# Performance work log

Measured on AMD Instinct MI355X. Metric: run time of the kernel, lower is better.

Reference implementation:

```python
import jax, jax.numpy as jnp
import numpy as np

B, N, D = 4, 8192, 128
H = 4 * D  # exp_factor * features
EPS = 1e-5


def layer_norm(x):
    # fresh nn.LayerNorm each call -> weight=1, bias=0 (no learned affine)
    mu = jnp.mean(x, axis=-1, keepdims=True)
    var = jnp.var(x, axis=-1, keepdims=True)
    return (x - mu) * jax.lax.rsqrt(var + EPS)


def setup_inputs() -> dict:
    key = jax.random.key(0)
    ks = jax.random.split(key, 8)
    x = jax.random.normal(ks[0], (B, N, D), dtype=jnp.float32)
    adj = jax.random.uniform(ks[1], (N, N), dtype=jnp.float32)
    attn_mask = jnp.ones((1,), dtype=jnp.int32)  # unused (torch masked_fill result discarded)
    pad_mask = jnp.ones((1,), dtype=jnp.int32)   # unused
    # FFN params (torch Linear default init scale ~ 1/sqrt(fan_in))
    w1 = jax.random.normal(ks[2], (D, H), dtype=jnp.float32) / np.sqrt(D)
    b1 = jnp.zeros((H,), dtype=jnp.float32)
    w2 = jax.random.normal(ks[3], (H, D), dtype=jnp.float32) / np.sqrt(H)
    b2 = jnp.zeros((D,), dtype=jnp.float32)
    return {"x": x, "adj": adj, "attn_mask": attn_mask, "pad_mask": pad_mask,
            "w1": w1, "b1": b1, "w2": w2, "b2": b2, "dim": 128}


def reference(x, adj, attn_mask, pad_mask, w1, b1, w2, b2, dim):
    # Sublayer 0: x + InrAwaSA(LN(x))
    h = layer_norm(x)                               # [B,N,D]
    # adj is provided -> scores = dense adj, shared across batch.
    # NOTE: masks are no-ops in the source (masked_fill not in-place).
    prob = jax.nn.softmax(adj, axis=-1)             # [N,N]
    attn_out = jnp.einsum('nm,bmd->bnd', prob, h)   # [B,N,D]
    x1 = x + attn_out
    # Sublayer 1: x1 + FFN(LN(x1))
    h1 = layer_norm(x1)
    ffn = jnp.maximum(h1 @ w1 + b1, 0.0) @ w2 + b2
    return x1 + ffn
```

## Files before the change

kernel.cpp:

```cpp
#include <hip/hip_runtime.h>
#include <hip/hip_bf16.h>

typedef __attribute__((ext_vector_type(8))) short bh8;
typedef __attribute__((ext_vector_type(4))) float fx4;
typedef __attribute__((ext_vector_type(8))) int i32x8;
typedef __attribute__((ext_vector_type(4))) int i32x4;

typedef const __attribute__((address_space(1))) unsigned int* gas_p;
typedef __attribute__((address_space(3))) unsigned int* las_p;

#define MFMA(a, b, c) __builtin_amdgcn_mfma_f32_16x16x32_bf16((a), (b), (c), 0, 0, 0)
#define MFMAS(a, b, c) __builtin_amdgcn_mfma_scale_f32_16x16x128_f8f6f4( \
    (a), (b), (c), 0, 0, 0, 0x7f7f7f7f, 0, 0x7f7f7f7f)

__device__ __forceinline__ unsigned short f2bf(float f) {
  unsigned u = __builtin_bit_cast(unsigned, f);
  u += 0x7fff + ((u >> 16) & 1);
  return (unsigned short)(u >> 16);
}

__device__ __forceinline__ float bflo2f(unsigned u) { return __builtin_bit_cast(float, u << 16); }

__device__ __forceinline__ void gld16(const void* g, void* l) {
  __builtin_amdgcn_global_load_lds((gas_p)g, (las_p)l, 16, 0, 0);
}

__global__ __launch_bounds__(256) void transpose_weights(const float* __restrict__ w1,
                                                         const float* __restrict__ w2,
                                                         unsigned short* __restrict__ w1t,
                                                         unsigned short* __restrict__ w2t) {
  const int tgl = blockIdx.x * 256 + threadIdx.x;
  { const int h = tgl >> 7, d = tgl & 127; w1t[tgl] = f2bf(w1[d * 512 + h]); }
  { const int d = tgl >> 9, h = tgl & 511; w2t[tgl] = f2bf(w2[h * 128 + d]); }
}

__global__ __launch_bounds__(256) void ln1_transpose(const float* __restrict__ x,
                                                     unsigned char* __restrict__ ht) {
  const int t = threadIdx.x, lane = t & 63, w = t >> 6;
  const int mt = blockIdx.x, b = blockIdx.y;
  __shared__ unsigned short tile[128 * 64];
  const float* xb = x + ((size_t)b * 8192 + (size_t)mt * 64) * 128;
  for (int it = 0; it < 16; ++it) {
    const int r = w * 16 + it;
    const float2 v = *(const float2*)(xb + r * 128 + lane * 2);
    float s = v.x + v.y, s2 = v.x * v.x + v.y * v.y;
    #pragma unroll
    for (int o = 1; o < 64; o <<= 1) { s += __shfl_xor(s, o); s2 += __shfl_xor(s2, o); }
    const float mean = s * 0.0078125f;
    const float var = s2 * 0.0078125f - mean * mean;
    const float rstd = rsqrtf(var + 1e-5f);
    const int mc = r >> 3, ml = r & 7;
    const int d0 = lane * 2, d1 = d0 + 1;
    tile[d0 * 64 + ((mc ^ (d0 & 7)) << 3) + ml] = f2bf((v.x - mean) * rstd);
    tile[d1 * 64 + ((mc ^ (d1 & 7)) << 3) + ml] = f2bf((v.y - mean) * rstd);
  }
  __syncthreads();
  unsigned char* hb = ht + (size_t)b * 128 * 8192 + (size_t)mt * 64;
  #pragma unroll
  for (int i = 0; i < 4; ++i) {
    const int idx = i * 256 + t;
    const int d = idx >> 3, mc = idx & 7;
    const bh8 vv = *(const bh8*)(tile + d * 64 + ((mc ^ (d & 7)) << 3));
    int lo = 0, hi = 0;
    lo = __builtin_amdgcn_cvt_pk_fp8_f32(bflo2f((unsigned short)vv[0]),
                                         bflo2f((unsigned short)vv[1]), lo, false);
    lo = __builtin_amdgcn_cvt_pk_fp8_f32(bflo2f((unsigned short)vv[2]),
                                         bflo2f((unsigned short)vv[3]), lo, true);
    hi = __builtin_amdgcn_cvt_pk_fp8_f32(bflo2f((unsigned short)vv[4]),
                                         bflo2f((unsigned short)vv[5]), hi, false);
    hi = __builtin_amdgcn_cvt_pk_fp8_f32(bflo2f((unsigned short)vv[6]),
                                         bflo2f((unsigned short)vv[7]), hi, true);
    *(uint2*)(hb + (size_t)d * 8192 + mc * 8) = (uint2){(unsigned)lo, (unsigned)hi};
  }
}

__global__ __launch_bounds__(256, 2) void fused_attn(const float* __restrict__ adj,
                                                     const unsigned char* __restrict__ ht,
                                                     unsigned short* __restrict__ pbuf,
                                                     float* __restrict__ sden) {
  const int tid = threadIdx.x, lane = tid & 63, wn = tid >> 6;
  const int mt = blockIdx.x, z = blockIdx.y;
  const int kbase = z * 2048;

  __shared__ unsigned char Al[64 * 128];

  fx4 acc[4][8];
  #pragma unroll
  for (int i = 0; i < 4; ++i)
    #pragma unroll
    for (int j = 0; j < 8; ++j) acc[i][j] = (fx4){0.f, 0.f, 0.f, 0.f};

  i32x8 afr[4];

  const int ar = tid >> 2, aq = tid & 3;
  const float* aroot = adj + (size_t)(mt * 64 + ar) * 8192 + kbase;
  float sacc = 0.f;
  float4 a4[8];
  unsigned pk[8];

  auto issueAdj = [&](int tau) {
    #pragma unroll
    for (int j = 0; j < 8; ++j)
      a4[j] = *(const float4*)(aroot + tau * 128 + j * 16 + aq * 4);
  };
  auto expCvt = [&]() {
    #pragma unroll
    for (int j = 0; j < 8; ++j) {
      const float e0 = __expf(a4[j].x), e1 = __expf(a4[j].y);
      const float e2 = __expf(a4[j].z), e3 = __expf(a4[j].w);
      sacc += (e0 + e1) + (e2 + e3);
      int d = 0;
      d = __builtin_amdgcn_cvt_pk_fp8_f32(e0, e1, d, false);
      d = __builtin_amdgcn_cvt_pk_fp8_f32(e2, e3, d, true);
      pk[j] = (unsigned)d;
    }
  };
  auto writeA = [&]() {
    #pragma unroll
    for (int j = 0; j < 8; ++j)
      *(unsigned*)&Al[ar * 128 + ((j ^ (ar & 7)) << 4) + aq * 4] = pk[j];
  };
  auto ldAall = [&]() {
    #pragma unroll
    for (int mf = 0; mf < 4; ++mf) {
      const int rr = mf * 16 + (lane & 15);
      const int gb = (lane >> 4) * 2;
      const unsigned char* base = &Al[rr * 128];
      const i32x4 lo = *(const i32x4*)(base + ((gb ^ (rr & 7)) << 4));
      const i32x4 hi = *(const i32x4*)(base + (((gb + 1) ^ (rr & 7)) << 4));
      afr[mf] = (i32x8){lo.x, lo.y, lo.z, lo.w, hi.x, hi.y, hi.z, hi.w};
    }
  };

  issueAdj(0);
  expCvt();
  writeA();
  asm volatile("s_waitcnt lgkmcnt(0)" ::: "memory");
  __builtin_amdgcn_sched_barrier(0);
  __builtin_amdgcn_s_barrier();
  __builtin_amdgcn_sched_barrier(0);

  for (int tt = 0; tt < 16; ++tt) {
    ldAall();
    if (tt < 15) issueAdj(tt + 1);
    asm volatile("s_waitcnt lgkmcnt(0)" ::: "memory");
    __builtin_amdgcn_sched_barrier(0);
    __builtin_amdgcn_s_barrier();
    __builtin_amdgcn_sched_barrier(0);

    const unsigned char* bb = ht + kbase + tt * 128 + (size_t)(lane >> 4) * 32;
    #pragma unroll
    for (int p = 0; p < 8; ++p) {
      const int c = wn * 128 + p * 16 + (lane & 15);
      const unsigned char* cb = bb + (size_t)c * 8192;
      const i32x4 blo = *(const i32x4*)(cb);
      const i32x4 bhi = *(const i32x4*)(cb + 16);
      const i32x8 bfr = (i32x8){blo.x, blo.y, blo.z, blo.w, bhi.x, bhi.y, bhi.z, bhi.w};
      #pragma unroll
      for (int mf = 0; mf < 4; ++mf)
        acc[mf][p] = MFMAS(afr[mf], bfr, acc[mf][p]);
    }

    if (tt < 15) {
      expCvt();
      writeA();
      asm volatile("s_waitcnt lgkmcnt(0)" ::: "memory");
      __builtin_amdgcn_sched_barrier(0);
    }
    __builtin_amdgcn_s_barrier();
    __builtin_amdgcn_sched_barrier(0);
  }

  sacc += __shfl_xor(sacc, 1);
  sacc += __shfl_xor(sacc, 2);
  if (aq == 0) sden[(size_t)z * 8192 + mt * 64 + ar] = sacc;

  unsigned short* po = pbuf + (size_t)z * 8192 * 512;
  #pragma unroll
  for (int mf = 0; mf < 4; ++mf)
    #pragma unroll
    for (int nf = 0; nf < 8; ++nf) {
      const int col = wn * 128 + nf * 16 + (lane & 15);
      #pragma unroll
      for (int q = 0; q < 4; ++q) {
        const int row = mt * 64 + mf * 16 + (lane >> 4) * 4 + q;
        po[(size_t)row * 512 + col] = f2bf(acc[mf][nf][q]);
      }
    }
}

#define SWZ16(ks, r) (((((ks) & 7) ^ ((r) & 7)) | ((ks) & 8)))
__global__ __launch_bounds__(512) void ln_ffn_kernel(const float* __restrict__ x,
                                                     const unsigned short* __restrict__ pbuf,
                                                     const float* __restrict__ sden,
                                                     const unsigned short* __restrict__ w1t,
                                                     const unsigned short* __restrict__ w2t,
                                                     const float* __restrict__ b1,
                                                     const float* __restrict__ b2,
                                                     float* __restrict__ out) {
  const int t = threadIdx.x, lane = t & 63, w = t >> 6;
  const int wr = w >> 1, wc = w & 1;
  const int row0 = blockIdx.x * 128;
  __shared__ unsigned short As[128 * 128];
  __shared__ unsigned short W1c[128 * 128];
  __shared__ unsigned short W2c[128 * 128];
  __shared__ unsigned short Ts[128 * 128];

  auto stageW1 = [&](int hc) {
    #pragma unroll
    for (int i = 0; i < 4; ++i) {
      const int idx = i * 512 + t;
      const int row = idx >> 4, kc = idx & 15;
      const int kcs = (kc & 8) | ((kc & 7) ^ (row & 7));
      gld16(w1t + (size_t)(hc * 128 + row) * 128 + kcs * 8, W1c + (idx & ~63) * 8);
    }
  };
  auto stageW2 = [&](int hc) {
    #pragma unroll
    for (int i = 0; i < 4; ++i) {
      const int idx = i * 512 + t;
      const int row = idx >> 4, kc = idx & 15;
      const int kcs = (kc & 8) | ((kc & 7) ^ (row & 7));
      gld16(w2t + (size_t)row * 512 + hc * 128 + kcs * 8, W2c + (idx & ~63) * 8);
    }
  };

  stageW1(0); stageW2(0);

  const int r = t >> 2, q = t & 3, c0 = q * 32;
  const int rowg = row0 + r;
  const int bb = rowg >> 13, nn = rowg & 8191;
  float xv[32];
  {
    const float den = sden[nn] + sden[8192 + nn] + sden[16384 + nn] + sden[24576 + nn];
    const float rinv = 1.f / den;
    const float* xp = x + (size_t)rowg * 128 + c0;
    #pragma unroll
    for (int j = 0; j < 8; ++j) {
      const float4 v4 = *(const float4*)(xp + 4 * j);
      xv[4 * j] = v4.x; xv[4 * j + 1] = v4.y; xv[4 * j + 2] = v4.z; xv[4 * j + 3] = v4.w;
    }
    #pragma unroll
    for (int z = 0; z < 4; ++z) {
      const unsigned short* pp = pbuf + ((size_t)z * 8192 + nn) * 512 + bb * 128 + c0;
      #pragma unroll
      for (int j = 0; j < 4; ++j) {
        const bh8 pv = *(const bh8*)(pp + 8 * j);
        #pragma unroll
        for (int e = 0; e < 8; ++e) xv[8 * j + e] += bflo2f((unsigned short)pv[e]) * rinv;
      }
    }
  }
  float s = 0.f, s2 = 0.f;
  #pragma unroll
  for (int j = 0; j < 32; ++j) { s += xv[j]; s2 += xv[j] * xv[j]; }
  s += __shfl_xor(s, 1); s2 += __shfl_xor(s2, 1);
  s += __shfl_xor(s, 2); s2 += __shfl_xor(s2, 2);
  const float mean = s * 0.0078125f;
  const float var = s2 * 0.0078125f - mean * mean;
  const float rstd = rsqrtf(var + 1e-5f);
  #pragma unroll
  for (int j = 0; j < 4; ++j) {
    const int g = q * 4 + j;
    bh8 pk;
    #pragma unroll
    for (int e = 0; e < 8; ++e) pk[e] = (short)f2bf((xv[8 * j + e] - mean) * rstd);
    *(bh8*)(As + r * 128 + SWZ16(g, r) * 8) = pk;
  }
  __syncthreads();

  fx4 accO[2][4];
  #pragma unroll
  for (int i = 0; i < 2; ++i)
    #pragma unroll
    for (int j = 0; j < 4; ++j) accO[i][j] = (fx4){0.f, 0.f, 0.f, 0.f};

  for (int hc = 0; hc < 4; ++hc) {
    if (hc > 0) stageW2(hc);
    fx4 accT[2][4];
    #pragma unroll
    for (int i = 0; i < 2; ++i)
      #pragma unroll
      for (int j = 0; j < 4; ++j) accT[i][j] = (fx4){0.f, 0.f, 0.f, 0.f};
    #pragma unroll
    for (int kk = 0; kk < 4; ++kk) {
      const int ks = kk * 4 + (lane >> 4);
      bh8 af[2], bfr[4];
      #pragma unroll
      for (int f = 0; f < 2; ++f) {
        const int ra = wr * 32 + f * 16 + (lane & 15);
        af[f] = *(const bh8*)(As + ra * 128 + SWZ16(ks, ra) * 8);
      }
      #pragma unroll
      for (int f = 0; f < 4; ++f) {
        const int rb = wc * 64 + f * 16 + (lane & 15);
        bfr[f] = *(const bh8*)(W1c + rb * 128 + SWZ16(ks, rb) * 8);
      }
      #pragma unroll
      for (int fm = 0; fm < 2; ++fm)
        #pragma unroll
        for (int fn = 0; fn < 4; ++fn) accT[fm][fn] = MFMA(af[fm], bfr[fn], accT[fm][fn]);
    }
    #pragma unroll
    for (int fm = 0; fm < 2; ++fm)
      #pragma unroll
      for (int fn = 0; fn < 4; ++fn) {
        const int col = wc * 64 + fn * 16 + (lane & 15);
        const float bv = b1[hc * 128 + col];
        const int c = col >> 3;
        #pragma unroll
        for (int qq = 0; qq < 4; ++qq) {
          const int row = wr * 32 + fm * 16 + (lane >> 4) * 4 + qq;
          float vv = accT[fm][fn][qq] + bv;
          vv = fmaxf(vv, 0.f);
          Ts[row * 128 + SWZ16(c, row) * 8 + (col & 7)] = f2bf(vv);
        }
      }
    __syncthreads();
    if (hc < 3) {
      stageW1(hc + 1);
    } else {
      float* dst = (r < 64) ? (float*)As + r * 128 + c0 : (float*)W1c + (r - 64) * 128 + c0;
      #pragma unroll
      for (int j = 0; j < 8; ++j)
        *(float4*)(dst + 4 * j) =
            (float4){xv[4 * j], xv[4 * j + 1], xv[4 * j + 2], xv[4 * j + 3]};
    }
    #pragma unroll
    for (int kk = 0; kk < 4; ++kk) {
      const int ks = kk * 4 + (lane >> 4);
      bh8 af[2], bfr[4];
      #pragma unroll
      for (int f = 0; f < 2; ++f) {
        const int ra = wr * 32 + f * 16 + (lane & 15);
        af[f] = *(const bh8*)(Ts + ra * 128 + SWZ16(ks, ra) * 8);
      }
      #pragma unroll
      for (int f = 0; f < 4; ++f) {
        const int rb = wc * 64 + f * 16 + (lane & 15);
        bfr[f] = *(const bh8*)(W2c + rb * 128 + SWZ16(ks, rb) * 8);
      }
      #pragma unroll
      for (int fm = 0; fm < 2; ++fm)
        #pragma unroll
        for (int fn = 0; fn < 4; ++fn) accO[fm][fn] = MFMA(af[fm], bfr[fn], accO[fm][fn]);
    }
    __syncthreads();
  }

  const float* x1a = (const float*)As;
  const float* x1b = (const float*)W1c;
  float* op = out + (size_t)row0 * 128;
  #pragma unroll
  for (int fm = 0; fm < 2; ++fm)
    #pragma unroll
    for (int fn = 0; fn < 4; ++fn) {
      const int col = wc * 64 + fn * 16 + (lane & 15);
      const float bv = b2[col];
      #pragma unroll
      for (int qq = 0; qq < 4; ++qq) {
        const int row = wr * 32 + fm * 16 + (lane >> 4) * 4 + qq;
        const float x1v = (row < 64) ? x1a[row * 128 + col] : x1b[(row - 64) * 128 + col];
        op[row * 128 + col] = x1v + accO[fm][fn][qq] + bv;
      }
    }
}

extern "C" void kernel_launch(void* const* d_in, const int* in_sizes, int n_in,
                              void* d_out, int out_size, void* d_ws, size_t ws_size,
                              hipStream_t stream) {
  const float* x   = (const float*)d_in[0];
  const float* adj = (const float*)d_in[1];
  const float* w1  = (const float*)d_in[4];
  const float* b1  = (const float*)d_in[5];
  const float* w2  = (const float*)d_in[6];
  const float* b2  = (const float*)d_in[7];
  float* out = (float*)d_out;

  char* p = (char*)d_ws;
  unsigned short* w1t  = (unsigned short*)p; p += (size_t)512 * 128 * 2;
  unsigned short* w2t  = (unsigned short*)p; p += (size_t)128 * 512 * 2;
  unsigned char*  ht   = (unsigned char*)p;  p += (size_t)4 * 128 * 8192;
  unsigned short* pbuf = (unsigned short*)p; p += (size_t)4 * 8192 * 512 * 2;
  float*          sden = (float*)p;          p += (size_t)4 * 8192 * 4;

  transpose_weights<<<256, 256, 0, stream>>>(w1, w2, w1t, w2t);
  ln1_transpose<<<dim3(128, 4), 256, 0, stream>>>(x, ht);
  fused_attn<<<dim3(128, 4), 256, 0, stream>>>(adj, ht, pbuf, sden);
  ln_ffn_kernel<<<256, 512, 0, stream>>>(x, pbuf, sden, w1t, w2t, b1, b2, out);
}
```

Measured before the change: 180.4 us.

## Stage fp8 B tile into LDS via global_load_lds with swizzled layout

The fp8 transposed-h operand is now copied into a 64KB swizzled LDS buffer with direct global-to-LDS loads, one tile ahead, instead of each wave reading it straight from global memory inside the MFMA loop. The adj load layout changes so each thread owns 32 contiguous floats, letting the A tile be written to LDS with two 16-byte stores. This aims to remove strided global latency from the MFMA loop and cut LDS store instructions. The cost is 64KB more shared memory per block, which may limit occupancy with launch_bounds(256,2), plus a full vmcnt(0) wait each iteration.

```diff
diff --git a/kernel.cpp b/kernel.cpp
--- a/kernel.cpp
+++ b/kernel.cpp
@@ -83,6 +83,7 @@
   const int kbase = z * 2048;
 
   __shared__ unsigned char Al[64 * 128];
+  __shared__ unsigned char Bl[512 * 128];
 
   fx4 acc[4][8];
   #pragma unroll
@@ -101,7 +102,7 @@
   auto issueAdj = [&](int tau) {
     #pragma unroll
     for (int j = 0; j < 8; ++j)
-      a4[j] = *(const float4*)(aroot + tau * 128 + j * 16 + aq * 4);
+      a4[j] = *(const float4*)(aroot + tau * 128 + aq * 32 + j * 4);
   };
   auto expCvt = [&]() {
     #pragma unroll
@@ -116,9 +117,19 @@
     }
   };
   auto writeA = [&]() {
-    #pragma unroll
-    for (int j = 0; j < 8; ++j)
-      *(unsigned*)&Al[ar * 128 + ((j ^ (ar & 7)) << 4) + aq * 4] = pk[j];
+    const i32x4 w0 = (i32x4){(int)pk[0], (int)pk[1], (int)pk[2], (int)pk[3]};
+    const i32x4 w1 = (i32x4){(int)pk[4], (int)pk[5], (int)pk[6], (int)pk[7]};
+    *(i32x4*)&Al[ar * 128 + (((aq * 2) ^ (ar & 7)) << 4)] = w0;
+    *(i32x4*)&Al[ar * 128 + (((aq * 2 + 1) ^ (ar & 7)) << 4)] = w1;
+  };
+  auto stageB = [&](int tau) {
+    #pragma unroll
+    for (int j = 0; j < 16; ++j) {
+      const int idx = j * 256 + tid;
+      const int col = idx >> 3, g = idx & 7;
+      gld16(ht + (size_t)col * 8192 + kbase + tau * 128 + ((g ^ (col & 7)) << 4),
+            Bl + idx * 16);
+    }
   };
   auto ldAall = [&]() {
     #pragma unroll
@@ -135,7 +146,8 @@
   issueAdj(0);
   expCvt();
   writeA();
-  asm volatile("s_waitcnt lgkmcnt(0)" ::: "memory");
+  stageB(0);
+  asm volatile("s_waitcnt lgkmcnt(0) vmcnt(0)" ::: "memory");
   __builtin_amdgcn_sched_barrier(0);
   __builtin_amdgcn_s_barrier();
   __builtin_amdgcn_sched_barrier(0);
@@ -143,32 +155,34 @@
   for (int tt = 0; tt < 16; ++tt) {
     ldAall();
     if (tt < 15) issueAdj(tt + 1);
+
+    #pragma unroll
+    for (int nf = 0; nf < 8; ++nf) {
+      const int c = wn * 128 + nf * 16 + (lane & 15);
+      const int gb = (lane >> 4) * 2;
+      const unsigned char* cb = &Bl[c * 128];
+      const i32x4 blo = *(const i32x4*)(cb + ((gb ^ (c & 7)) << 4));
+      const i32x4 bhi = *(const i32x4*)(cb + (((gb + 1) ^ (c & 7)) << 4));
+      const i32x8 bfr = (i32x8){blo.x, blo.y, blo.z, blo.w, bhi.x, bhi.y, bhi.z, bhi.w};
+      #pragma unroll
+      for (int mf = 0; mf < 4; ++mf)
+        acc[mf][nf] = MFMAS(afr[mf], bfr, acc[mf][nf]);
+    }
+
     asm volatile("s_waitcnt lgkmcnt(0)" ::: "memory");
     __builtin_amdgcn_sched_barrier(0);
     __builtin_amdgcn_s_barrier();
     __builtin_amdgcn_sched_barrier(0);
 
-    const unsigned char* bb = ht + kbase + tt * 128 + (size_t)(lane >> 4) * 32;
-    #pragma unroll
-    for (int p = 0; p < 8; ++p) {
-      const int c = wn * 128 + p * 16 + (lane & 15);
-      const unsigned char* cb = bb + (size_t)c * 8192;
-      const i32x4 blo = *(const i32x4*)(cb);
-      const i32x4 bhi = *(const i32x4*)(cb + 16);
-      const i32x8 bfr = (i32x8){blo.x, blo.y, blo.z, blo.w, bhi.x, bhi.y, bhi.z, bhi.w};
-      #pragma unroll
-      for (int mf = 0; mf < 4; ++mf)
-        acc[mf][p] = MFMAS(afr[mf], bfr, acc[mf][p]);
-    }
-
     if (tt < 15) {
+      stageB(tt + 1);
       expCvt();
       writeA();
-      asm volatile("s_waitcnt lgkmcnt(0)" ::: "memory");
+      asm volatile("s_waitcnt lgkmcnt(0) vmcnt(0)" ::: "memory");
       __builtin_amdgcn_sched_barrier(0);
-    }
-    __builtin_amdgcn_s_barrier();
-    __builtin_amdgcn_sched_barrier(0);
+      __builtin_amdgcn_s_barrier();
+      __builtin_amdgcn_sched_barrier(0);
+    }
   }
 
   sacc += __shfl_xor(sacc, 1);
```

Result: faster. 151.1 us (-16.2%).

## Pre-swizzle fp8 attention B operand into MFMA fragment layout and overlap with barrier

Applied to the files above, without the earlier changes.

The LN1 output is written straight into a fragment-major layout, so each lane in fused_attn reads a contiguous 32-byte chunk per MFMA fragment instead of strided rows that are 8 KB apart. The B-fragment loads and MFMAs now run before the LDS barrier, which overlaps them with the wait. One barrier is dropped on the last iteration. The adj loads are reordered so each thread reads 32 contiguous floats and writes LDS with two 16-byte stores instead of eight 4-byte ones. The aim is better global coalescing and fewer LDS instructions, at the cost of more complex index math in the producer kernel.

```diff
diff --git a/kernel.cpp b/kernel.cpp
--- a/kernel.cpp
+++ b/kernel.cpp
@@ -35,7 +35,7 @@
 }
 
 __global__ __launch_bounds__(256) void ln1_transpose(const float* __restrict__ x,
-                                                     unsigned char* __restrict__ ht) {
+                                                     unsigned char* __restrict__ htf) {
   const int t = threadIdx.x, lane = t & 63, w = t >> 6;
   const int mt = blockIdx.x, b = blockIdx.y;
   __shared__ unsigned short tile[128 * 64];
@@ -55,7 +55,6 @@
     tile[d1 * 64 + ((mc ^ (d1 & 7)) << 3) + ml] = f2bf((v.y - mean) * rstd);
   }
   __syncthreads();
-  unsigned char* hb = ht + (size_t)b * 128 * 8192 + (size_t)mt * 64;
   #pragma unroll
   for (int i = 0; i < 4; ++i) {
     const int idx = i * 256 + t;
@@ -70,12 +69,16 @@
                                          bflo2f((unsigned short)vv[5]), hi, false);
     hi = __builtin_amdgcn_cvt_pk_fp8_f32(bflo2f((unsigned short)vv[6]),
                                          bflo2f((unsigned short)vv[7]), hi, true);
-    *(uint2*)(hb + (size_t)d * 8192 + mc * 8) = (uint2){(unsigned)lo, (unsigned)hi};
+    const int col = b * 128 + d;
+    const int k0 = mt * 64 + mc * 8;
+    const int frag = (k0 >> 7) * 32 + (col >> 4);
+    const int off = ((col & 15) + 16 * ((k0 >> 5) & 3)) * 32 + (k0 & 31);
+    *(uint2*)(htf + (size_t)frag * 2048 + off) = (uint2){(unsigned)lo, (unsigned)hi};
   }
 }
 
 __global__ __launch_bounds__(256, 2) void fused_attn(const float* __restrict__ adj,
-                                                     const unsigned char* __restrict__ ht,
+                                                     const unsigned char* __restrict__ htf,
                                                      unsigned short* __restrict__ pbuf,
                                                      float* __restrict__ sden) {
   const int tid = threadIdx.x, lane = tid & 63, wn = tid >> 6;
@@ -101,7 +104,7 @@
   auto issueAdj = [&](int tau) {
     #pragma unroll
     for (int j = 0; j < 8; ++j)
-      a4[j] = *(const float4*)(aroot + tau * 128 + j * 16 + aq * 4);
+      a4[j] = *(const float4*)(aroot + tau * 128 + aq * 32 + j * 4);
   };
   auto expCvt = [&]() {
     #pragma unroll
@@ -116,9 +119,10 @@
     }
   };
   auto writeA = [&]() {
-    #pragma unroll
-    for (int j = 0; j < 8; ++j)
-      *(unsigned*)&Al[ar * 128 + ((j ^ (ar & 7)) << 4) + aq * 4] = pk[j];
+    const i32x4 w0 = (i32x4){(int)pk[0], (int)pk[1], (int)pk[2], (int)pk[3]};
+    const i32x4 w1 = (i32x4){(int)pk[4], (int)pk[5], (int)pk[6], (int)pk[7]};
+    *(i32x4*)&Al[ar * 128 + (((aq * 2) ^ (ar & 7)) << 4)] = w0;
+    *(i32x4*)&Al[ar * 128 + (((aq * 2 + 1) ^ (ar & 7)) << 4)] = w1;
   };
   auto ldAall = [&]() {
     #pragma unroll
@@ -143,32 +147,33 @@
   for (int tt = 0; tt < 16; ++tt) {
     ldAall();
     if (tt < 15) issueAdj(tt + 1);
+
+    const int gkt = z * 16 + tt;
+    const unsigned char* fb = htf + ((size_t)gkt * 32 + wn * 8) * 2048 + lane * 32;
+    #pragma unroll
+    for (int nf = 0; nf < 8; ++nf) {
+      const unsigned char* fp = fb + nf * 2048;
+      const i32x4 blo = *(const i32x4*)(fp);
+      const i32x4 bhi = *(const i32x4*)(fp + 16);
+      const i32x8 bfr = (i32x8){blo.x, blo.y, blo.z, blo.w, bhi.x, bhi.y, bhi.z, bhi.w};
+      #pragma unroll
+      for (int mf = 0; mf < 4; ++mf)
+        acc[mf][nf] = MFMAS(afr[mf], bfr, acc[mf][nf]);
+    }
+
     asm volatile("s_waitcnt lgkmcnt(0)" ::: "memory");
     __builtin_amdgcn_sched_barrier(0);
     __builtin_amdgcn_s_barrier();
     __builtin_amdgcn_sched_barrier(0);
-
-    const unsigned char* bb = ht + kbase + tt * 128 + (size_t)(lane >> 4) * 32;
-    #pragma unroll
-    for (int p = 0; p < 8; ++p) {
-      const int c = wn * 128 + p * 16 + (lane & 15);
-      const unsigned char* cb = bb + (size_t)c * 8192;
-      const i32x4 blo = *(const i32x4*)(cb);
-      const i32x4 bhi = *(const i32x4*)(cb + 16);
-      const i32x8 bfr = (i32x8){blo.x, blo.y, blo.z, blo.w, bhi.x, bhi.y, bhi.z, bhi.w};
-      #pragma unroll
-      for (int mf = 0; mf < 4; ++mf)
-        acc[mf][p] = MFMAS(afr[mf], bfr, acc[mf][p]);
-    }
 
     if (tt < 15) {
       expCvt();
       writeA();
       asm volatile("s_waitcnt lgkmcnt(0)" ::: "memory");
       __builtin_amdgcn_sched_barrier(0);
-    }
-    __builtin_amdgcn_s_barrier();
-    __builtin_amdgcn_sched_barrier(0);
+      __builtin_amdgcn_s_barrier();
+      __builtin_amdgcn_sched_barrier(0);
+    }
   }
 
   sacc += __shfl_xor(sacc, 1);
@@ -380,12 +385,12 @@
   char* p = (char*)d_ws;
   unsigned short* w1t  = (unsigned short*)p; p += (size_t)512 * 128 * 2;
   unsigned short* w2t  = (unsigned short*)p; p += (size_t)128 * 512 * 2;
-  unsigned char*  ht   = (unsigned char*)p;  p += (size_t)4 * 128 * 8192;
+  unsigned char*  htf  = (unsigned char*)p;  p += (size_t)4 * 128 * 8192;
   unsigned short* pbuf = (unsigned short*)p; p += (size_t)4 * 8192 * 512 * 2;
   float*          sden = (float*)p;          p += (size_t)4 * 8192 * 4;
 
   transpose_weights<<<256, 256, 0, stream>>>(w1, w2, w1t, w2t);
-  ln1_transpose<<<dim3(128, 4), 256, 0, stream>>>(x, ht);
-  fused_attn<<<dim3(128, 4), 256, 0, stream>>>(adj, ht, pbuf, sden);
+  ln1_transpose<<<dim3(128, 4), 256, 0, stream>>>(x, htf);
+  fused_attn<<<dim3(128, 4), 256, 0, stream>>>(adj, htf, pbuf, sden);
   ln_ffn_kernel<<<256, 512, 0, stream>>>(x, pbuf, sden, w1t, w2t, b1, b2, out);
 }
```

Result: faster. 162.9 us (-9.7%).
